# Performance work log

Hardware: AMD Instinct MI355X
Metric: run time of the kernel (lower is better)

## Reference

```python
import jax, jax.numpy as jnp
import numpy as np

SEQ_LEN = 20   # fixed by the 18/19/20-position loop in get_each_word_feature
EMB = 768
FEAT = 512
EPS = 1e-12    # F.normalize eps


def _conv_relu(x, W, b):
    # x: [bs, L, 768]; W: [K, 768, C]; b: [C]
    # Equivalent to Conv2d(1, C, (K, 768)) on x.unsqueeze(1), then ReLU+squeeze.
    K = W.shape[0]
    L = x.shape[1]
    out = b
    for j in range(K):  # K in {1,2,3}: tiny static loop
        out = out + jnp.einsum('bld,dc->blc', x[:, j:L - K + 1 + j], W[j])
    return jax.nn.relu(out)  # [bs, L-K+1, C]


def _l2norm(x, axis):
    n = jnp.sqrt(jnp.sum(x * x, axis=axis, keepdims=True))
    return x / jnp.maximum(n, EPS)


def setup_inputs() -> dict:
    key = jax.random.key(0)
    ks = jax.random.split(key, 10)
    bs = 4096
    s = 0.02
    return {
        'words_emb': jax.random.normal(ks[0], (bs, SEQ_LEN, EMB), jnp.float32),
        'sent_emb': jax.random.normal(ks[1], (bs, EMB), jnp.float32),
        'W1': jax.random.normal(ks[2], (1, EMB, FEAT), jnp.float32) * s,
        'b1': jnp.zeros((FEAT,), jnp.float32),
        'W2': jax.random.normal(ks[3], (2, EMB, FEAT), jnp.float32) * s,
        'b2': jnp.zeros((FEAT,), jnp.float32),
        'W3': jax.random.normal(ks[4], (3, EMB, FEAT), jnp.float32) * s,
        'b3': jnp.zeros((FEAT,), jnp.float32),
        'Wp': jax.random.normal(ks[5], (EMB, FEAT), jnp.float32) * s,
        'bp': jnp.zeros((FEAT,), jnp.float32),
    }


def reference(words_emb, sent_emb, W1, b1, W2, b2, W3, b3, Wp, bp):
    # sentence projection (ProjectionHead.forward applies only the Linear)
    sent = sent_emb @ Wp + bp                       # [bs, C]

    # Bert_Word_Mapping: three 1D convs over tokens, kernel widths 1/2/3
    a = _conv_relu(words_emb, W1, b1)               # [bs, 20, C]
    b_ = _conv_relu(words_emb, W2, b2)              # [bs, 19, C]
    c = _conv_relu(words_emb, W3, b3)               # [bs, 18, C]

    # get_each_word_feature, vectorized: positional max over available convs.
    # ReLU outputs are >= 0, so zero-padding short sequences makes the
    # elementwise max reproduce the original per-position stack+amax exactly.
    b_pad = jnp.pad(b_, ((0, 0), (0, 1), (0, 0)))   # [bs, 20, C]
    c_pad = jnp.pad(c, ((0, 0), (0, 2), (0, 0)))    # [bs, 20, C]
    code = jnp.maximum(jnp.maximum(a, b_pad), c_pad)
    code = _l2norm(code, axis=2)                    # normalize over feature dim
    words_out = jnp.transpose(code, (0, 2, 1))      # [bs, C, 20]

    # get_word_feature: global max-pool over token dim, mean of 3, L2 norm
    pooled = (a.max(axis=1) + b_.max(axis=1) + c.max(axis=1)) / 3.0  # [bs, C]
    word_vector = _l2norm(pooled, axis=1)

    return (words_out, word_vector, sent)
```

## Files before the change

kernel.cpp:

```cpp
#include <hip/hip_runtime.h>
#include <hip/hip_bf16.h>
#include <stdint.h>

typedef __bf16 bf16_t;
typedef __bf16 bf16x8 __attribute__((ext_vector_type(8)));
typedef float f32x4 __attribute__((ext_vector_type(4)));

#define BS       4096
#define SEQ      20
#define SEQP     22
#define EMB      768
#define FEAT     512
#define KA       2304
#define WV_BASE   (41943040L)
#define SENT_BASE (44040192L)

#define BT_OFF    0L
#define WPT_OFF   7077888L
#define SENTX_OFF 7864320L
#define XPAD_OFF  14155776L
#define WS_MIN    111673344L
#define WS_FULL   404226048L

__device__ __forceinline__ void async_copy16(void* lds, const void* g) {
  __builtin_amdgcn_global_load_lds(
      (__attribute__((address_space(1))) void*)(void*)g,
      (__attribute__((address_space(3))) void*)lds,
      16, 0, 0);
}

__global__ void pack_xpad(const float* __restrict__ words, bf16_t* __restrict__ Xpad) {
  long idx4 = ((long)blockIdx.x * blockDim.x + threadIdx.x) * 4;
  long row = idx4 / EMB;
  int  d   = (int)(idx4 % EMB);
  long b   = row / SEQP;
  int  r   = (int)(row % SEQP);
  ushort4 o;
  if (r < SEQ) {
    float4 v = *(const float4*)(words + ((b * SEQ + r) * EMB + d));
    o.x = __builtin_bit_cast(unsigned short, (bf16_t)v.x);
    o.y = __builtin_bit_cast(unsigned short, (bf16_t)v.y);
    o.z = __builtin_bit_cast(unsigned short, (bf16_t)v.z);
    o.w = __builtin_bit_cast(unsigned short, (bf16_t)v.w);
  } else {
    o.x = 0; o.y = 0; o.z = 0; o.w = 0;
  }
  *(ushort4*)(&Xpad[idx4]) = o;
}

__global__ void pack_sent(const float* __restrict__ sent, bf16_t* __restrict__ Xs) {
  long idx4 = ((long)blockIdx.x * blockDim.x + threadIdx.x) * 4;
  float4 v = *(const float4*)(sent + idx4);
  ushort4 o;
  o.x = __builtin_bit_cast(unsigned short, (bf16_t)v.x);
  o.y = __builtin_bit_cast(unsigned short, (bf16_t)v.y);
  o.z = __builtin_bit_cast(unsigned short, (bf16_t)v.z);
  o.w = __builtin_bit_cast(unsigned short, (bf16_t)v.w);
  *(ushort4*)(&Xs[idx4]) = o;
}

__global__ void pack_bt(const float* __restrict__ W1, const float* __restrict__ W2,
                        const float* __restrict__ W3, bf16_t* __restrict__ Bt) {
  long idx = (long)blockIdx.x * blockDim.x + threadIdx.x;
  int n = (int)(idx / KA), k = (int)(idx % KA);
  int g = n >> 9, c = n & 511;
  int j = k / EMB, d = k % EMB;
  float v = 0.f;
  if (j <= g) {
    const float* W = (g == 0) ? W1 : ((g == 1) ? W2 : W3);
    v = W[((long)j * EMB + d) * FEAT + c];
  }
  Bt[idx] = (bf16_t)v;
}

__global__ void pack_wpt(const float* __restrict__ Wp, bf16_t* __restrict__ Wpt) {
  long idx = (long)blockIdx.x * blockDim.x + threadIdx.x;
  int n = (int)(idx / EMB), k = (int)(idx % EMB);
  Wpt[idx] = (bf16_t)Wp[(long)k * FEAT + n];
}

__global__ __launch_bounds__(256, 2)
void gemm_sent(const bf16_t* __restrict__ A, const bf16_t* __restrict__ Bt,
               const float* __restrict__ bias, float* __restrict__ S) {
  __shared__ bf16_t As[128 * 64];
  __shared__ bf16_t Bs[128 * 64];

  const int tid  = threadIdx.x;
  const int lane = tid & 63;
  const int w    = tid >> 6;
  const int m0   = blockIdx.x * 128;
  const int n0t  = blockIdx.y * 128;

  long agbase[4], bgbase[4];
  int  ldsoff[4];
  #pragma unroll
  for (int i = 0; i < 4; i++) {
    int r = w * 32 + i * 8 + (lane >> 3);
    int cg = (lane & 7) ^ (r & 7);
    agbase[i] = (long)(m0 + r) * EMB + cg * 8;
    bgbase[i] = (long)(n0t + r) * EMB + cg * 8;
    ldsoff[i] = (w * 32 + i * 8) * 64;
  }

  const int wm = w >> 1, wn = w & 1;
  const int q = lane >> 4, ln = lane & 15;
  int aoff[4][2], boff[4][2];
  #pragma unroll
  for (int t = 0; t < 4; t++) {
    int ra = wm * 64 + t * 16 + ln;
    int rb = wn * 64 + t * 16 + ln;
    #pragma unroll
    for (int ks = 0; ks < 2; ks++) {
      int c = ks * 4 + q;
      aoff[t][ks] = ra * 64 + ((c ^ (ra & 7)) * 8);
      boff[t][ks] = rb * 64 + ((c ^ (rb & 7)) * 8);
    }
  }

  f32x4 acc[4][4];
  #pragma unroll
  for (int i = 0; i < 4; i++)
    #pragma unroll
    for (int j = 0; j < 4; j++) acc[i][j] = (f32x4)0.f;

  for (int kb = 0; kb < EMB; kb += 64) {
    #pragma unroll
    for (int i = 0; i < 4; i++) {
      async_copy16(&As[ldsoff[i]], A  + agbase[i] + kb);
      async_copy16(&Bs[ldsoff[i]], Bt + bgbase[i] + kb);
    }
    __syncthreads();
    #pragma unroll
    for (int ks = 0; ks < 2; ks++) {
      bf16x8 af[4], bfr[4];
      #pragma unroll
      for (int t = 0; t < 4; t++) af[t]  = *(const bf16x8*)&As[aoff[t][ks]];
      #pragma unroll
      for (int t = 0; t < 4; t++) bfr[t] = *(const bf16x8*)&Bs[boff[t][ks]];
      #pragma unroll
      for (int mt = 0; mt < 4; mt++)
        #pragma unroll
        for (int nt = 0; nt < 4; nt++)
          acc[mt][nt] = __builtin_amdgcn_mfma_f32_16x16x32_bf16(af[mt], bfr[nt], acc[mt][nt], 0, 0, 0);
    }
    __syncthreads();
  }

  #pragma unroll
  for (int nt = 0; nt < 4; nt++) {
    int c = n0t + wn * 64 + nt * 16 + ln;
    float bv = bias[c];
    #pragma unroll
    for (int mt = 0; mt < 4; mt++) {
      int mrow = m0 + wm * 64 + mt * 16 + q * 4;
      #pragma unroll
      for (int v = 0; v < 4; v++)
        S[(long)(mrow + v) * FEAT + c] = acc[mt][nt][v] + bv;
    }
  }
}


#define MFMA16(BASE, A0, A1, A2, A3, B0, B1, B2, B3)                                        \
  acc[(BASE)+0][0] = __builtin_amdgcn_mfma_f32_16x16x32_bf16(A0, B0, acc[(BASE)+0][0], 0, 0, 0); \
  acc[(BASE)+0][1] = __builtin_amdgcn_mfma_f32_16x16x32_bf16(A0, B1, acc[(BASE)+0][1], 0, 0, 0); \
  acc[(BASE)+0][2] = __builtin_amdgcn_mfma_f32_16x16x32_bf16(A0, B2, acc[(BASE)+0][2], 0, 0, 0); \
  acc[(BASE)+0][3] = __builtin_amdgcn_mfma_f32_16x16x32_bf16(A0, B3, acc[(BASE)+0][3], 0, 0, 0); \
  acc[(BASE)+1][0] = __builtin_amdgcn_mfma_f32_16x16x32_bf16(A1, B0, acc[(BASE)+1][0], 0, 0, 0); \
  acc[(BASE)+1][1] = __builtin_amdgcn_mfma_f32_16x16x32_bf16(A1, B1, acc[(BASE)+1][1], 0, 0, 0); \
  acc[(BASE)+1][2] = __builtin_amdgcn_mfma_f32_16x16x32_bf16(A1, B2, acc[(BASE)+1][2], 0, 0, 0); \
  acc[(BASE)+1][3] = __builtin_amdgcn_mfma_f32_16x16x32_bf16(A1, B3, acc[(BASE)+1][3], 0, 0, 0); \
  acc[(BASE)+2][0] = __builtin_amdgcn_mfma_f32_16x16x32_bf16(A2, B0, acc[(BASE)+2][0], 0, 0, 0); \
  acc[(BASE)+2][1] = __builtin_amdgcn_mfma_f32_16x16x32_bf16(A2, B1, acc[(BASE)+2][1], 0, 0, 0); \
  acc[(BASE)+2][2] = __builtin_amdgcn_mfma_f32_16x16x32_bf16(A2, B2, acc[(BASE)+2][2], 0, 0, 0); \
  acc[(BASE)+2][3] = __builtin_amdgcn_mfma_f32_16x16x32_bf16(A2, B3, acc[(BASE)+2][3], 0, 0, 0); \
  acc[(BASE)+3][0] = __builtin_amdgcn_mfma_f32_16x16x32_bf16(A3, B0, acc[(BASE)+3][0], 0, 0, 0); \
  acc[(BASE)+3][1] = __builtin_amdgcn_mfma_f32_16x16x32_bf16(A3, B1, acc[(BASE)+3][1], 0, 0, 0); \
  acc[(BASE)+3][2] = __builtin_amdgcn_mfma_f32_16x16x32_bf16(A3, B2, acc[(BASE)+3][2], 0, 0, 0); \
  acc[(BASE)+3][3] = __builtin_amdgcn_mfma_f32_16x16x32_bf16(A3, B3, acc[(BASE)+3][3], 0, 0, 0);

__global__ __launch_bounds__(512, 2)
void gemm8(const bf16_t* __restrict__ Axp, const bf16_t* __restrict__ Bt,
           const float* __restrict__ bias1, const float* __restrict__ bias2,
           const float* __restrict__ bias3, bf16_t* __restrict__ P, int Mtot) {
  __shared__ bf16_t smem[65536];

  const int tid  = threadIdx.x;
  const int lane = tid & 63, w = tid >> 6;
  const int wm = w >> 2, wn = w & 3;
  const int ln = lane & 15, q = lane >> 4;
  const int wbase = w * 512;

  const int nx   = gridDim.x;
  const int nwg  = nx * 6;
  const int orig = blockIdx.y * nx + blockIdx.x;
  const int wgid = (orig & 7) * (nwg >> 3) + (orig >> 3);
  const int bx = wgid / 6, by = wgid % 6;
  const int m0  = bx * 256;
  const int n0t = by * 256;
  const int g   = by >> 1;
  const int NT  = 12 * (g + 1);

  long aSrc0, aSrc1, bSrc0, bSrc1;
  {
    int pair = (tid >> 3);
    int u    = (tid & 7) ^ (pair & 7);
    int row  = pair * 2 + (u >> 2);
    int c    = u & 3;
    int m    = m0 + row;
    aSrc0 = ((long)(m / SEQ) * SEQP + (m % SEQ)) * EMB + c * 8;
    bSrc0 = (long)(n0t + row) * KA + c * 8;
    pair += 64;
    u   = (tid & 7) ^ (pair & 7);
    row = pair * 2 + (u >> 2);
    c   = u & 3;
    m   = m0 + row;
    aSrc1 = ((long)(m / SEQ) * SEQP + (m % SEQ)) * EMB + c * 8;
    bSrc1 = (long)(n0t + row) * KA + c * 8;
  }

  auto stA = [&](int buf, int ks, int kb) {
    const int rb = buf * 32768 + ks * 8192;
    async_copy16(&smem[rb + wbase],        Axp + aSrc0 + kb + ks * 32);
    async_copy16(&smem[rb + 4096 + wbase], Axp + aSrc1 + kb + ks * 32);
  };
  auto stB = [&](int buf, int ks, int kb) {
    const int rb = buf * 32768 + 16384 + ks * 8192;
    async_copy16(&smem[rb + wbase],        Bt + bSrc0 + kb + ks * 32);
    async_copy16(&smem[rb + 4096 + wbase], Bt + bSrc1 + kb + ks * 32);
  };

  int aoff[2][4], boff[4];
  #pragma unroll
  for (int mh = 0; mh < 2; mh++)
    #pragma unroll
    for (int t4 = 0; t4 < 4; t4++) {
      int r = wm * 128 + mh * 64 + t4 * 16 + ln;
      int slot = (q | ((r & 1) << 2)) ^ ((r >> 1) & 7);
      aoff[mh][t4] = (r >> 1) * 64 + slot * 8;
    }
  #pragma unroll
  for (int nf = 0; nf < 4; nf++) {
    int r = wn * 64 + nf * 16 + ln;
    int slot = (q | ((r & 1) << 2)) ^ ((r >> 1) & 7);
    boff[nf] = (r >> 1) * 64 + slot * 8;
  }

  f32x4 acc[8][4];
  #pragma unroll
  for (int i = 0; i < 8; i++)
    #pragma unroll
    for (int j = 0; j < 4; j++) acc[i][j] = (f32x4)0.f;

  stA(0, 0, 0);
  stA(0, 1, 0);
  stB(0, 0, 0);
  stB(0, 1, 0);
  stB(1, 0, 64);
  stA(1, 0, 64);
  stB(1, 1, 64);
  asm volatile("s_waitcnt vmcnt(6)" ::: "memory");
  __builtin_amdgcn_s_barrier();

  for (int t = 0; t < NT; ++t) {
    const int cb  = (t & 1) << 15;
    const int ab0 = cb, ab1 = cb + 8192;
    const int bb0 = cb + 16384, bb1 = cb + 24576;
    const int nb  = (t & 1) ^ 1;

    bf16x8 aP0 = *(const bf16x8*)&smem[ab0 + aoff[0][0]];
    bf16x8 aP1 = *(const bf16x8*)&smem[ab0 + aoff[0][1]];
    bf16x8 aP2 = *(const bf16x8*)&smem[ab0 + aoff[0][2]];
    bf16x8 aP3 = *(const bf16x8*)&smem[ab0 + aoff[0][3]];
    bf16x8 bP0 = *(const bf16x8*)&smem[bb0 + boff[0]];
    bf16x8 bP1 = *(const bf16x8*)&smem[bb0 + boff[1]];
    bf16x8 bP2 = *(const bf16x8*)&smem[bb0 + boff[2]];
    bf16x8 bP3 = *(const bf16x8*)&smem[bb0 + boff[3]];

    {
      bf16x8 aN0 = *(const bf16x8*)&smem[ab0 + aoff[1][0]];
      bf16x8 aN1 = *(const bf16x8*)&smem[ab0 + aoff[1][1]];
      bf16x8 aN2 = *(const bf16x8*)&smem[ab0 + aoff[1][2]];
      bf16x8 aN3 = *(const bf16x8*)&smem[ab0 + aoff[1][3]];
      if (t + 1 < NT) stA(nb, 1, (t + 1) * 64);
      __builtin_amdgcn_sched_barrier(0);
      __builtin_amdgcn_s_setprio(1);
      MFMA16(0, aP0, aP1, aP2, aP3, bP0, bP1, bP2, bP3)
      __builtin_amdgcn_s_setprio(0);
      __builtin_amdgcn_s_barrier();

      bf16x8 aQ0 = *(const bf16x8*)&smem[ab1 + aoff[0][0]];
      bf16x8 aQ1 = *(const bf16x8*)&smem[ab1 + aoff[0][1]];
      bf16x8 aQ2 = *(const bf16x8*)&smem[ab1 + aoff[0][2]];
      bf16x8 aQ3 = *(const bf16x8*)&smem[ab1 + aoff[0][3]];
      bf16x8 bN0 = *(const bf16x8*)&smem[bb1 + boff[0]];
      bf16x8 bN1 = *(const bf16x8*)&smem[bb1 + boff[1]];
      bf16x8 bN2 = *(const bf16x8*)&smem[bb1 + boff[2]];
      bf16x8 bN3 = *(const bf16x8*)&smem[bb1 + boff[3]];
      if (t + 2 < NT) stB(t & 1, 0, (t + 2) * 64);
      __builtin_amdgcn_sched_barrier(0);
      __builtin_amdgcn_s_setprio(1);
      MFMA16(4, aN0, aN1, aN2, aN3, bP0, bP1, bP2, bP3)
      __builtin_amdgcn_s_setprio(0);
      __builtin_amdgcn_s_barrier();

      bf16x8 aR0 = *(const bf16x8*)&smem[ab1 + aoff[1][0]];
      bf16x8 aR1 = *(const bf16x8*)&smem[ab1 + aoff[1][1]];
      bf16x8 aR2 = *(const bf16x8*)&smem[ab1 + aoff[1][2]];
      bf16x8 aR3 = *(const bf16x8*)&smem[ab1 + aoff[1][3]];
      if (t + 2 < NT) stA(t & 1, 0, (t + 2) * 64);
      __builtin_amdgcn_sched_barrier(0);
      __builtin_amdgcn_s_setprio(1);
      MFMA16(0, aQ0, aQ1, aQ2, aQ3, bN0, bN1, bN2, bN3)
      __builtin_amdgcn_s_setprio(0);
      __builtin_amdgcn_s_barrier();

      if (t + 2 < NT) stB(t & 1, 1, (t + 2) * 64);
      __builtin_amdgcn_sched_barrier(0);
      __builtin_amdgcn_s_setprio(1);
      MFMA16(4, aR0, aR1, aR2, aR3, bN0, bN1, bN2, bN3)
      __builtin_amdgcn_s_setprio(0);
      if (t + 2 < NT)      { asm volatile("s_waitcnt vmcnt(4)" ::: "memory"); }
      else if (t + 1 < NT) { asm volatile("s_waitcnt vmcnt(0)" ::: "memory"); }
      if (t + 1 < NT) __builtin_amdgcn_s_barrier();
    }
  }

  const float* bias = (g == 0) ? bias1 : ((g == 1) ? bias2 : bias3);
  const int gc0 = (by & 1) * 256;
  #pragma unroll
  for (int nf = 0; nf < 4; nf++) {
    int c = gc0 + wn * 64 + nf * 16 + ln;
    float bv = bias[c];
    #pragma unroll
    for (int mf = 0; mf < 8; mf++) {
      int mrow = m0 + wm * 128 + mf * 16 + q * 4;
      #pragma unroll
      for (int v = 0; v < 4; v++) {
        int m = mrow + v;
        int l = m % SEQ;
        float val = acc[mf][nf][v] + bv;
        val = val > 0.f ? val : 0.f;
        if (l >= SEQ - g) val = 0.f;
        P[((long)g * Mtot + m) * FEAT + c] = (bf16_t)val;
      }
    }
  }
}

__global__ __launch_bounds__(256)
void epilogue_k(const bf16_t* __restrict__ P, float* __restrict__ out, int b0, int Mtot) {
  const int bl = blockIdx.x;
  const long b = b0 + bl;
  const int t = threadIdx.x;
  const int lane = t & 63, w = t >> 6;
  const int c0 = t * 2;

  float code[SEQ][2];
  #pragma unroll
  for (int l = 0; l < SEQ; l++) { code[l][0] = 0.f; code[l][1] = 0.f; }
  float mg[3][2];

  #pragma unroll
  for (int gg = 0; gg < 3; gg++) {
    float mx0 = 0.f, mx1 = 0.f;
    #pragma unroll
    for (int l = 0; l < SEQ; l++) {
      uint32_t u = *(const uint32_t*)&P[((long)gg * Mtot + (long)bl * SEQ + l) * FEAT + c0];
      float v0 = __builtin_bit_cast(float, u << 16);
      float v1 = __builtin_bit_cast(float, u & 0xffff0000u);
      code[l][0] = fmaxf(code[l][0], v0);
      code[l][1] = fmaxf(code[l][1], v1);
      mx0 = fmaxf(mx0, v0); mx1 = fmaxf(mx1, v1);
    }
    mg[gg][0] = mx0; mg[gg][1] = mx1;
  }

  __shared__ float red[SEQ][4];
  __shared__ float redp[4];

  #pragma unroll
  for (int l = 0; l < SEQ; l++) {
    float s = code[l][0] * code[l][0] + code[l][1] * code[l][1];
    #pragma unroll
    for (int off = 32; off; off >>= 1) s += __shfl_xor(s, off, 64);
    if (lane == 0) red[l][w] = s;
  }
  float p0 = (mg[0][0] + mg[1][0] + mg[2][0]) * (1.f / 3.f);
  float p1 = (mg[0][1] + mg[1][1] + mg[2][1]) * (1.f / 3.f);
  float sp = p0 * p0 + p1 * p1;
  #pragma unroll
  for (int off = 32; off; off >>= 1) sp += __shfl_xor(sp, off, 64);
  if (lane == 0) redp[w] = sp;
  __syncthreads();

  float rnorm[SEQ];
  #pragma unroll
  for (int l = 0; l < SEQ; l++) {
    float s = red[l][0] + red[l][1] + red[l][2] + red[l][3];
    rnorm[l] = 1.f / fmaxf(sqrtf(s), 1e-12f);
  }
  float sP = redp[0] + redp[1] + redp[2] + redp[3];
  float rnp = 1.f / fmaxf(sqrtf(sP), 1e-12f);

  #pragma unroll
  for (int cc = 0; cc < 2; cc++) {
    long base = b * (FEAT * SEQ) + (long)(c0 + cc) * SEQ;
    #pragma unroll
    for (int l0 = 0; l0 < SEQ; l0 += 4) {
      float4 v;
      v.x = code[l0 + 0][cc] * rnorm[l0 + 0];
      v.y = code[l0 + 1][cc] * rnorm[l0 + 1];
      v.z = code[l0 + 2][cc] * rnorm[l0 + 2];
      v.w = code[l0 + 3][cc] * rnorm[l0 + 3];
      *(float4*)&out[base + l0] = v;
    }
  }
  out[WV_BASE + b * FEAT + c0]     = p0 * rnp;
  out[WV_BASE + b * FEAT + c0 + 1] = p1 * rnp;
}

extern "C" void kernel_launch(void* const* d_in, const int* in_sizes, int n_in,
                              void* d_out, int out_size, void* d_ws, size_t ws_size,
                              hipStream_t stream) {
  const float* words = (const float*)d_in[0];
  const float* sent  = (const float*)d_in[1];
  const float* W1 = (const float*)d_in[2];
  const float* b1 = (const float*)d_in[3];
  const float* W2 = (const float*)d_in[4];
  const float* b2 = (const float*)d_in[5];
  const float* W3 = (const float*)d_in[6];
  const float* b3 = (const float*)d_in[7];
  const float* Wp = (const float*)d_in[8];
  const float* bp = (const float*)d_in[9];
  float* out = (float*)d_out;
  char* ws = (char*)d_ws;

  int CBr, NCH;
  if (ws_size >= (size_t)WS_FULL)     { CBr = 4096; NCH = 1; }
  else if (ws_size >= (size_t)WS_MIN) { CBr = 1024; NCH = 4; }
  else return;

  const int Mtot = CBr * SEQ;
  bf16_t* Bt    = (bf16_t*)(ws + BT_OFF);
  bf16_t* Wpt   = (bf16_t*)(ws + WPT_OFF);
  bf16_t* sentX = (bf16_t*)(ws + SENTX_OFF);
  bf16_t* Xpad  = (bf16_t*)(ws + XPAD_OFF);
  bf16_t* P     = (bf16_t*)(ws + XPAD_OFF + (long)CBr * SEQP * EMB * 2);

  pack_bt<<<13824, 256, 0, stream>>>(W1, W2, W3, Bt);
  pack_wpt<<<1536, 256, 0, stream>>>(Wp, Wpt);
  pack_sent<<<3072, 256, 0, stream>>>(sent, sentX);
  gemm_sent<<<dim3(32, 4), 256, 0, stream>>>(sentX, Wpt, bp, out + SENT_BASE);

  for (int ch = 0; ch < NCH; ch++) {
    int b0 = ch * CBr;
    pack_xpad<<<(CBr * SEQP * EMB) / 1024, 256, 0, stream>>>(words + (long)b0 * SEQ * EMB, Xpad);
    gemm8<<<dim3(Mtot / 256, 6), 512, 0, stream>>>(Xpad, Bt, b1, b2, b3, P, Mtot);
    epilogue_k<<<CBr, 256, 0, stream>>>(P, out, b0, Mtot);
  }
}
```

Baseline: 919.1 us.

## Unroll GEMM main loop by two with prefetched fragments and heaviest-first block order

Unrolls the GEMM k-loop two tiles at a time with constant LDS buffer offsets. The first fragment set of the next tile is loaded right after the barrier at the end of each tile, so the loop no longer pays an LDS load bubble at the top. The grid is made one-dimensional and ordered so that blocks with the longest K (the 3-wide conv group) are dispatched first, which should shrink the tail. Wait counts change to vmcnt(6), and the peeled final tiles need careful bookkeeping of the outstanding loads.

```diff
diff --git a/kernel.cpp b/kernel.cpp
--- a/kernel.cpp
+++ b/kernel.cpp
@@ -179,6 +179,45 @@
   acc[(BASE)+3][2] = __builtin_amdgcn_mfma_f32_16x16x32_bf16(A3, B2, acc[(BASE)+3][2], 0, 0, 0); \
   acc[(BASE)+3][3] = __builtin_amdgcn_mfma_f32_16x16x32_bf16(A3, B3, acc[(BASE)+3][3], 0, 0, 0);
 
+#define LDV(X)  (*(const bf16x8*)&smem[(X)])
+#define VM6     asm volatile("s_waitcnt vmcnt(6)" ::: "memory")
+#define VM0     asm volatile("s_waitcnt vmcnt(0)" ::: "memory")
+#define SBAR    __builtin_amdgcn_s_barrier()
+#define SCB     __builtin_amdgcn_sched_barrier(0)
+#define PRI(x)  __builtin_amdgcn_s_setprio(x)
+
+#define TILE(AB0, AB1, BB0, BB1, NAB0, NBB0, ST1, ST2, ST3, ST4, WAITC, DOTOP)      \
+  {                                         \
+    aN0 = LDV((AB0) + aoff[1][0]); aN1 = LDV((AB0) + aoff[1][1]);                   \
+    aN2 = LDV((AB0) + aoff[1][2]); aN3 = LDV((AB0) + aoff[1][3]);                   \
+    ST1; SCB; PRI(1);                                                               \
+    MFMA16(0, aP0, aP1, aP2, aP3, bP0, bP1, bP2, bP3)                               \
+    PRI(0); SBAR;                                                                   \
+                                    \
+    aQ0 = LDV((AB1) + aoff[0][0]); aQ1 = LDV((AB1) + aoff[0][1]);                   \
+    aQ2 = LDV((AB1) + aoff[0][2]); aQ3 = LDV((AB1) + aoff[0][3]);                   \
+    bN0 = LDV((BB1) + boff[0]); bN1 = LDV((BB1) + boff[1]);                         \
+    bN2 = LDV((BB1) + boff[2]); bN3 = LDV((BB1) + boff[3]);                         \
+    ST2; SCB; PRI(1);                                                               \
+    MFMA16(4, aN0, aN1, aN2, aN3, bP0, bP1, bP2, bP3)                               \
+    PRI(0); SBAR;                                                                   \
+                                            \
+    aR0 = LDV((AB1) + aoff[1][0]); aR1 = LDV((AB1) + aoff[1][1]);                   \
+    aR2 = LDV((AB1) + aoff[1][2]); aR3 = LDV((AB1) + aoff[1][3]);                   \
+    ST3; SCB; PRI(1);                                                               \
+    MFMA16(0, aQ0, aQ1, aQ2, aQ3, bN0, bN1, bN2, bN3)                               \
+    PRI(0); SBAR;                                                                   \
+                       \
+    ST4; SCB; PRI(1);                                                               \
+    MFMA16(4, aR0, aR1, aR2, aR3, bN0, bN1, bN2, bN3)                               \
+    PRI(0); WAITC;                                                                  \
+    if (DOTOP) { SBAR; SCB;                                                         \
+      aP0 = LDV((NAB0) + aoff[0][0]); aP1 = LDV((NAB0) + aoff[0][1]);               \
+      aP2 = LDV((NAB0) + aoff[0][2]); aP3 = LDV((NAB0) + aoff[0][3]);               \
+      bP0 = LDV((NBB0) + boff[0]); bP1 = LDV((NBB0) + boff[1]);                     \
+      bP2 = LDV((NBB0) + boff[2]); bP3 = LDV((NBB0) + boff[3]); }                   \
+  }
+
 __global__ __launch_bounds__(512, 2)
 void gemm8(const bf16_t* __restrict__ Axp, const bf16_t* __restrict__ Bt,
            const float* __restrict__ bias1, const float* __restrict__ bias2,
@@ -191,15 +230,19 @@
   const int ln = lane & 15, q = lane >> 4;
   const int wbase = w * 512;
 
-  const int nx   = gridDim.x;
-  const int nwg  = nx * 6;
-  const int orig = blockIdx.y * nx + blockIdx.x;
-  const int wgid = (orig & 7) * (nwg >> 3) + (orig >> 3);
-  const int bx = wgid / 6, by = wgid % 6;
-  const int m0  = bx * 256;
-  const int n0t = by * 256;
-  const int g   = by >> 1;
-  const int NT  = 12 * (g + 1);
+  const int S    = gridDim.x / 3;
+  const int orig = blockIdx.x;
+  const int seg  = orig / S;
+  const int g    = 2 - seg;
+  const int idx  = orig - seg * S;
+  const int wg   = (idx & 7) * (S >> 3) + (idx >> 3);
+  const int half = S >> 1;
+  const int nhalf = (wg >= half) ? 1 : 0;
+  const int bx   = wg - nhalf * half;
+  const int m0   = bx * 256;
+  const int n0t  = g * 512 + nhalf * 256;
+  const int gc0  = nhalf * 256;
+  const int NT   = 12 * (g + 1);
 
   long aSrc0, aSrc1, bSrc0, bSrc1;
   {
@@ -252,6 +295,10 @@
     #pragma unroll
     for (int j = 0; j < 4; j++) acc[i][j] = (f32x4)0.f;
 
+  bf16x8 aP0, aP1, aP2, aP3, bP0, bP1, bP2, bP3;
+  bf16x8 aN0, aN1, aN2, aN3, aQ0, aQ1, aQ2, aQ3;
+  bf16x8 bN0, bN1, bN2, bN3, aR0, aR1, aR2, aR3;
+
   stA(0, 0, 0);
   stA(0, 1, 0);
   stB(0, 0, 0);
@@ -259,75 +306,27 @@
   stB(1, 0, 64);
   stA(1, 0, 64);
   stB(1, 1, 64);
-  asm volatile("s_waitcnt vmcnt(6)" ::: "memory");
-  __builtin_amdgcn_s_barrier();
-
-  for (int t = 0; t < NT; ++t) {
-    const int cb  = (t & 1) << 15;
-    const int ab0 = cb, ab1 = cb + 8192;
-    const int bb0 = cb + 16384, bb1 = cb + 24576;
-    const int nb  = (t & 1) ^ 1;
-
-    bf16x8 aP0 = *(const bf16x8*)&smem[ab0 + aoff[0][0]];
-    bf16x8 aP1 = *(const bf16x8*)&smem[ab0 + aoff[0][1]];
-    bf16x8 aP2 = *(const bf16x8*)&smem[ab0 + aoff[0][2]];
-    bf16x8 aP3 = *(const bf16x8*)&smem[ab0 + aoff[0][3]];
-    bf16x8 bP0 = *(const bf16x8*)&smem[bb0 + boff[0]];
-    bf16x8 bP1 = *(const bf16x8*)&smem[bb0 + boff[1]];
-    bf16x8 bP2 = *(const bf16x8*)&smem[bb0 + boff[2]];
-    bf16x8 bP3 = *(const bf16x8*)&smem[bb0 + boff[3]];
-
-    {
-      bf16x8 aN0 = *(const bf16x8*)&smem[ab0 + aoff[1][0]];
-      bf16x8 aN1 = *(const bf16x8*)&smem[ab0 + aoff[1][1]];
-      bf16x8 aN2 = *(const bf16x8*)&smem[ab0 + aoff[1][2]];
-      bf16x8 aN3 = *(const bf16x8*)&smem[ab0 + aoff[1][3]];
-      if (t + 1 < NT) stA(nb, 1, (t + 1) * 64);
-      __builtin_amdgcn_sched_barrier(0);
-      __builtin_amdgcn_s_setprio(1);
-      MFMA16(0, aP0, aP1, aP2, aP3, bP0, bP1, bP2, bP3)
-      __builtin_amdgcn_s_setprio(0);
-      __builtin_amdgcn_s_barrier();
-
-      bf16x8 aQ0 = *(const bf16x8*)&smem[ab1 + aoff[0][0]];
-      bf16x8 aQ1 = *(const bf16x8*)&smem[ab1 + aoff[0][1]];
-      bf16x8 aQ2 = *(const bf16x8*)&smem[ab1 + aoff[0][2]];
-      bf16x8 aQ3 = *(const bf16x8*)&smem[ab1 + aoff[0][3]];
-      bf16x8 bN0 = *(const bf16x8*)&smem[bb1 + boff[0]];
-      bf16x8 bN1 = *(const bf16x8*)&smem[bb1 + boff[1]];
-      bf16x8 bN2 = *(const bf16x8*)&smem[bb1 + boff[2]];
-      bf16x8 bN3 = *(const bf16x8*)&smem[bb1 + boff[3]];
-      if (t + 2 < NT) stB(t & 1, 0, (t + 2) * 64);
-      __builtin_amdgcn_sched_barrier(0);
-      __builtin_amdgcn_s_setprio(1);
-      MFMA16(4, aN0, aN1, aN2, aN3, bP0, bP1, bP2, bP3)
-      __builtin_amdgcn_s_setprio(0);
-      __builtin_amdgcn_s_barrier();
-
-      bf16x8 aR0 = *(const bf16x8*)&smem[ab1 + aoff[1][0]];
-      bf16x8 aR1 = *(const bf16x8*)&smem[ab1 + aoff[1][1]];
-      bf16x8 aR2 = *(const bf16x8*)&smem[ab1 + aoff[1][2]];
-      bf16x8 aR3 = *(const bf16x8*)&smem[ab1 + aoff[1][3]];
-      if (t + 2 < NT) stA(t & 1, 0, (t + 2) * 64);
-      __builtin_amdgcn_sched_barrier(0);
-      __builtin_amdgcn_s_setprio(1);
-      MFMA16(0, aQ0, aQ1, aQ2, aQ3, bN0, bN1, bN2, bN3)
-      __builtin_amdgcn_s_setprio(0);
-      __builtin_amdgcn_s_barrier();
-
-      if (t + 2 < NT) stB(t & 1, 1, (t + 2) * 64);
-      __builtin_amdgcn_sched_barrier(0);
-      __builtin_amdgcn_s_setprio(1);
-      MFMA16(4, aR0, aR1, aR2, aR3, bN0, bN1, bN2, bN3)
-      __builtin_amdgcn_s_setprio(0);
-      if (t + 2 < NT)      { asm volatile("s_waitcnt vmcnt(4)" ::: "memory"); }
-      else if (t + 1 < NT) { asm volatile("s_waitcnt vmcnt(0)" ::: "memory"); }
-      if (t + 1 < NT) __builtin_amdgcn_s_barrier();
-    }
-  }
+  VM6;
+  SBAR; SCB;
+  aP0 = LDV(aoff[0][0]); aP1 = LDV(aoff[0][1]);
+  aP2 = LDV(aoff[0][2]); aP3 = LDV(aoff[0][3]);
+  bP0 = LDV(16384 + boff[0]); bP1 = LDV(16384 + boff[1]);
+  bP2 = LDV(16384 + boff[2]); bP3 = LDV(16384 + boff[3]);
+
+  int kA = 64, kB = 128;
+  for (int t = 0; t < NT - 3; t += 2) {
+    TILE(0, 8192, 16384, 24576, 32768, 49152,
+         stA(1, 1, kA), stB(0, 0, kB), stA(0, 0, kB), stB(0, 1, kB), VM6, 1)
+    TILE(32768, 40960, 49152, 57344, 0, 16384,
+         stA(0, 1, kA + 64), stB(1, 0, kB + 64), stA(1, 0, kB + 64), stB(1, 1, kB + 64), VM6, 1)
+    kA += 128; kB += 128;
+  }
+  TILE(0, 8192, 16384, 24576, 32768, 49152,
+       stA(1, 1, kA), , , , VM0, 1)
+  TILE(32768, 40960, 49152, 57344, 0, 16384,
+       , , , , , 0)
 
   const float* bias = (g == 0) ? bias1 : ((g == 1) ? bias2 : bias3);
-  const int gc0 = (by & 1) * 256;
   #pragma unroll
   for (int nf = 0; nf < 4; nf++) {
     int c = gc0 + wn * 64 + nf * 16 + ln;
@@ -456,7 +455,7 @@
   for (int ch = 0; ch < NCH; ch++) {
     int b0 = ch * CBr;
     pack_xpad<<<(CBr * SEQP * EMB) / 1024, 256, 0, stream>>>(words + (long)b0 * SEQ * EMB, Xpad);
-    gemm8<<<dim3(Mtot / 256, 6), 512, 0, stream>>>(Xpad, Bt, b1, b2, b3, P, Mtot);
+    gemm8<<<dim3(6 * (Mtot / 256)), 512, 0, stream>>>(Xpad, Bt, b1, b2, b3, P, Mtot);
     epilogue_k<<<CBr, 256, 0, stream>>>(P, out, b0, Mtot);
   }
 }
```

Measured after the change: 1.050 ms. +14.2%, slower.
